# Kernel tuning notes

Hardware: AMD Instinct MI355X
Metric: run time of the kernel (lower is better)

## Reference

```python
import jax, jax.numpy as jnp
import numpy as np

# SLAYER neuron / simulation hyperparameters (from network.yaml)
THETA = 10.0      # spike threshold
TAU_SR = 10.0     # SRM (PSP) kernel time constant [ms]
TAU_REF = 1.0     # refractory kernel time constant [ms]
SCALE_REF = 2.0   # refractory kernel scale
TS = 1.0          # simulation step [ms]
K_SRM = 100       # truncation length of SRM kernel (eps decays ~0 by 10*tau)
K_REF = 32        # truncation length of refractory kernel (tauRef=1 -> decays fast)


def _eps_kernel(tau, k):
    # eps(t) = (t/tau) * exp(1 - t/tau), eps(0) = 0  (SLAYER SRM alpha kernel)
    t = jnp.arange(k, dtype=jnp.float32) * TS
    return (t / tau) * jnp.exp(1.0 - t / tau)


def psp(x, kern):
    # Causal temporal filter: y[..., t] = sum_j kern[j] * x[..., t - j]
    B, N, T = x.shape
    lhs = x.reshape(B * N, 1, T)
    rhs = kern[::-1].reshape(1, 1, -1)  # lax.conv is cross-correlation -> flip
    y = jax.lax.conv_general_dilated(
        lhs, rhs, window_strides=(1,), padding=[(kern.shape[0] - 1, 0)],
        dimension_numbers=('NCH', 'OIH', 'NCH'))
    return y.reshape(B, N, T)


def spike(u, refk):
    # Sequential thresholding with refractory feedback (SLAYER spikeFunction fwd).
    # u: [B, N, T] membrane drive. State r: future refractory contributions.
    kr = refk.shape[0]
    refk_shift = jnp.concatenate([refk[1:], jnp.zeros((1,), refk.dtype)])

    def step(r, u_t):
        m = u_t + r[..., 0]                      # membrane potential at t
        s = (m >= THETA).astype(u_t.dtype)       # hard spike
        r_next = jnp.concatenate([r[..., 1:], jnp.zeros_like(r[..., :1])], -1) \
                 + s[..., None] * refk_shift     # add refractory response
        return r_next, s

    uT = jnp.moveaxis(u, -1, 0)                  # [T, B, N]
    r0 = jnp.zeros(uT.shape[1:] + (kr,), u.dtype)
    _, sT = jax.lax.scan(step, r0, uT)
    return jnp.moveaxis(sT, 0, -1) / TS          # [B, N, T]


def setup_inputs() -> dict:
    key = jax.random.key(0)
    k1, k2, k3 = jax.random.split(key, 3)
    B, NIN, NHID, NOUT, T = 32, 2048, 512, 10, 350
    spike_input = (jax.random.uniform(k1, (B, NIN, T)) < 0.05).astype(jnp.float32)
    W1 = jax.random.normal(k2, (NHID, NIN), dtype=jnp.float32) * 0.05
    W2 = jax.random.normal(k3, (NOUT, NHID), dtype=jnp.float32) * 0.05
    return {"spike_input": spike_input, "W1": W1, "W2": W2}


def reference(spike_input, W1, W2):
    srm = _eps_kernel(TAU_SR, K_SRM)
    refk = -SCALE_REF * THETA * _eps_kernel(TAU_REF, K_REF)
    # layer 1: psp -> dense -> spike
    a1 = jnp.einsum('bnt,mn->bmt', psp(spike_input, srm), W1)
    s1 = spike(a1, refk)
    # layer 2: psp -> dense -> spike
    a2 = jnp.einsum('bnt,mn->bmt', psp(s1, srm), W2)
    s2 = spike(a2, refk)
    return s2
```

## Files before the change

### kernel.cpp

```cpp
#include <hip/hip_runtime.h>
#include <stdint.h>

static constexpr int B  = 32;
static constexpr int T  = 350;
static constexpr int NIN = 2048;
static constexpr int NH  = 512;
static constexpr int NO  = 10;
static constexpr int BT  = B * T;

static constexpr float THETA = 10.0f;
static constexpr float BETA  = 0.36787944117144233f;
static constexpr float CREF  = 54.365636569180904707f;

static constexpr size_t OFF_W1T  = 0;
static constexpr size_t OFF_MASK = 4196352;
static constexpr size_t OFF_SRM  = 7063552;
static constexpr size_t OFF_Z1   = 7064576;
static constexpr size_t OFF_A1   = 30002176;
static constexpr size_t OFF_Z2   = OFF_A1;

__global__ void __launch_bounds__(256) k_prep(const float* __restrict__ x,
                                              const float* __restrict__ W1,
                                              float* __restrict__ W1T,
                                              uint64_t* __restrict__ mask,
                                              float* __restrict__ srm28) {
    int bid = blockIdx.x;
    if (bid < 1024) {
        __shared__ uint64_t tb[6][64];
        int b = bid >> 5, nblk = bid & 31;
        int wv = threadIdx.x >> 6, lane = threadIdx.x & 63;
        for (int nr = wv; nr < 64; nr += 4) {
            const float* xp = x + ((size_t)b * NIN + nblk * 64 + nr) * T;
            #pragma unroll
            for (int c = 0; c < 6; ++c) {
                int t = c * 64 + lane;
                float v = (t < T) ? xp[t] : 0.f;
                uint64_t mk = __ballot(v != 0.0f);
                if (lane == 0) tb[c][nr] = mk;
            }
        }
        __syncthreads();
        static const uint64_t AM[6] = {
            0x00000000FFFFFFFFull, 0x0000FFFF0000FFFFull, 0x00FF00FF00FF00FFull,
            0x0F0F0F0F0F0F0F0Full, 0x3333333333333333ull, 0x5555555555555555ull };
        for (int c = wv; c < 6; c += 4) {
            uint64_t w = tb[c][lane];
            #pragma unroll
            for (int i = 0; i < 6; ++i) {
                int s = 32 >> i;
                uint64_t A = AM[i];
                uint64_t y = __shfl_xor((unsigned long long)w, s);
                if ((lane & s) == 0) w = (w & A)  | ((y & A) << s);
                else                 w = (w & ~A) | ((y & ~A) >> s);
            }
            int t = c * 64 + lane;
            if (t < T) mask[((size_t)b * T + t) * 32 + nblk] = w;
        }
    } else if (bid < 2048) {
        __shared__ float tile[32][33];
        int idx = bid - 1024;
        int n0 = (idx & 63) * 32, m0 = (idx >> 6) * 32;
        int tx = threadIdx.x & 31, ty0 = threadIdx.x >> 5;
        #pragma unroll
        for (int i = 0; i < 4; ++i) {
            int ty = ty0 + 8 * i;
            tile[ty][tx] = W1[(size_t)(m0 + ty) * NIN + n0 + tx];
        }
        __syncthreads();
        #pragma unroll
        for (int i = 0; i < 4; ++i) {
            int ty = ty0 + 8 * i;
            W1T[(size_t)(n0 + ty) * NH + m0 + tx] = tile[tx][ty];
        }
    } else {
        int j = threadIdx.x;
        if (j < 192) {
            float v = 0.f;
            int i = j - 28;
            if (i >= 0 && i < 100) { float t = (float)i; v = (t * 0.1f) * expf(1.f - t * 0.1f); }
            srm28[j] = v;
        }
        for (int i = j; i < NH; i += 256) W1T[(size_t)2048 * NH + i] = 0.f;
    }
}

__global__ void __launch_bounds__(64) k_z1(const uint64_t* __restrict__ mask,
                                           const float* __restrict__ W1T,
                                           float* __restrict__ z1) {
    __shared__ alignas(8) uint16_t lst[288];
    int row = blockIdx.x, lane = threadIdx.x;
    const uint64_t* mrow = mask + (size_t)row * 32;
    uint64_t w = (lane < 32) ? mrow[lane] : 0ull;
    int cnt = __popcll(w);
    int pre = cnt;
    #pragma unroll
    for (int off = 1; off < 64; off <<= 1) {
        int v = __shfl_up(pre, off);
        if (lane >= off) pre += v;
    }
    int total = __shfl(pre, 63);
    int excl = pre - cnt;
    while (w) {
        int bit = __builtin_ctzll(w);
        w &= w - 1;
        lst[excl++] = (uint16_t)((lane << 6) + bit);
    }
    int padded = (total + 3) & ~3;
    if (lane < padded - total) lst[total + lane] = 2048;
    __syncthreads();

    const float4* W4 = (const float4*)W1T;
    float4 a0 = {0,0,0,0}, a1v = {0,0,0,0};
    int i0 = lane * 2, i1 = lane * 2 + 1;
    for (int k = 0; k < padded; k += 4) {
        ushort4 q = *(const ushort4*)(lst + k);
        const float4* p0 = W4 + (size_t)q.x * 128;
        const float4* p1 = W4 + (size_t)q.y * 128;
        const float4* p2 = W4 + (size_t)q.z * 128;
        const float4* p3 = W4 + (size_t)q.w * 128;
        float4 x0 = p0[i0], y0 = p0[i1];
        float4 x1 = p1[i0], y1 = p1[i1];
        float4 x2 = p2[i0], y2 = p2[i1];
        float4 x3 = p3[i0], y3 = p3[i1];
        a0.x += x0.x; a0.y += x0.y; a0.z += x0.z; a0.w += x0.w;
        a1v.x += y0.x; a1v.y += y0.y; a1v.z += y0.z; a1v.w += y0.w;
        a0.x += x1.x; a0.y += x1.y; a0.z += x1.z; a0.w += x1.w;
        a1v.x += y1.x; a1v.y += y1.y; a1v.z += y1.z; a1v.w += y1.w;
        a0.x += x2.x; a0.y += x2.y; a0.z += x2.z; a0.w += x2.w;
        a1v.x += y2.x; a1v.y += y2.y; a1v.z += y2.z; a1v.w += y2.w;
        a0.x += x3.x; a0.y += x3.y; a0.z += x3.z; a0.w += x3.w;
        a1v.x += y3.x; a1v.y += y3.y; a1v.z += y3.z; a1v.w += y3.w;
    }
    float4* zp = (float4*)(z1 + (size_t)row * NH);
    zp[i0] = a0; zp[i1] = a1v;
}

__global__ void __launch_bounds__(64) k_fir1(const float* __restrict__ src,
                                             float* __restrict__ dst,
                                             const float* __restrict__ srm28) {
    __shared__ float tb[192];
    int b = blockIdx.x, half = blockIdx.y, tg = blockIdx.z;
    int lane = threadIdx.x;
    for (int i = lane; i < 192; i += 64) tb[i] = srm28[i];
    __syncthreads();
    int t0 = tg * 16;
    int m = half * 256 + lane * 4;
    const float* sp = src + (size_t)b * T * NH + m;

    float4 acc[16];
    #pragma unroll
    for (int r = 0; r < 16; ++r) acc[r] = make_float4(0.f, 0.f, 0.f, 0.f);
    float c[16];
    #pragma unroll
    for (int r = 0; r < 16; ++r) c[r] = tb[r + 127];

    for (int o = 0; o < 8; ++o) {
        #pragma unroll
        for (int j = 0; j < 16; ++j) {
            int dd = o * 16 + j;
            int tau = t0 - 99 + dd;
            float4 v = make_float4(0.f, 0.f, 0.f, 0.f);
            if (tau >= 0 && tau < T) v = *(const float4*)(sp + (size_t)tau * NH);
            #pragma unroll
            for (int r = 0; r < 16; ++r) {
                acc[r].x += c[r] * v.x; acc[r].y += c[r] * v.y;
                acc[r].z += c[r] * v.z; acc[r].w += c[r] * v.w;
            }
            #pragma unroll
            for (int r = 15; r > 0; --r) c[r] = c[r - 1];
            int ci = 126 - dd;
            c[0] = tb[ci < 0 ? 0 : ci];
        }
    }
    #pragma unroll
    for (int r = 0; r < 16; ++r) {
        int t = t0 + r;
        if (t < T) *(float4*)(dst + ((size_t)b * T + t) * NH + m) = acc[r];
    }
}

template<int M, int LAYOUT_TM>
__global__ void k_scan_t(const float* __restrict__ u, float* __restrict__ s) {
    constexpr int CT = 16;
    constexpr int NC = (T + CT - 1) / CT;
    int tid = blockIdx.x * blockDim.x + threadIdx.x;
    if (tid >= B * M) return;
    int b = tid / M, m = tid - b * M;
    const float* up = u + (size_t)b * T * M + m;
    float cur[CT], nxt[CT];
    float A = 0.f, Bs = 0.f;
    #pragma unroll
    for (int j = 0; j < CT; ++j) cur[j] = up[(size_t)j * M];
    for (int c = 0; c < NC; ++c) {
        int t0 = c * CT;
        int nsteps = (T - t0 < CT) ? (T - t0) : CT;
        if (c + 1 < NC) {
            int t1 = t0 + CT;
            #pragma unroll
            for (int j = 0; j < CT; ++j) {
                int t = t1 + j;
                nxt[j] = (t < T) ? up[(size_t)t * M] : 0.f;
            }
        }
        float outbuf[CT];
        #pragma unroll
        for (int j = 0; j < CT; ++j) {
            if (j < nsteps) {
                float mem = cur[j] - CREF * Bs;
                float sp = (mem >= THETA) ? 1.0f : 0.0f;
                A = sp + BETA * A;
                Bs = BETA * (Bs + A);
                if (LAYOUT_TM) s[((size_t)b * T + (t0 + j)) * M + m] = sp;
                else           outbuf[j] = sp;
            }
        }
        if (!LAYOUT_TM) {
            #pragma unroll
            for (int j = 0; j < CT; ++j)
                if (j < nsteps) s[((size_t)(b * M + m)) * T + t0 + j] = outbuf[j];
        }
        #pragma unroll
        for (int j = 0; j < CT; ++j) cur[j] = nxt[j];
    }
}

__global__ void __launch_bounds__(64) k_z2(const float* __restrict__ s1,
                                           const float* __restrict__ W2,
                                           float* __restrict__ z2) {
    int row = blockIdx.x;
    int lane = threadIdx.x;
    const float* sp = s1 + (size_t)row * NH;
    float acc[NO];
    #pragma unroll
    for (int o = 0; o < NO; ++o) acc[o] = 0.f;
    for (int j = 0; j < 8; ++j) {
        int m = lane + 64 * j;
        float sv = sp[m];
        #pragma unroll
        for (int o = 0; o < NO; ++o) acc[o] += sv * W2[(size_t)o * NH + m];
    }
    #pragma unroll
    for (int o = 0; o < NO; ++o) {
        float v = acc[o];
        for (int off = 32; off > 0; off >>= 1) v += __shfl_down(v, off);
        if (lane == 0) z2[(size_t)row * NO + o] = v;
    }
}

__global__ void __launch_bounds__(256) k_fir2scan(const float* __restrict__ z2,
                                                  const float* __restrict__ srm28,
                                                  float* __restrict__ out) {
    __shared__ float tb[192];
    __shared__ float zb[350 * 11 + 16];
    __shared__ float ab[352 * 10];
    int b = blockIdx.x, tid = threadIdx.x;
    if (tid < 192) tb[tid] = srm28[tid];
    const float* zp = z2 + (size_t)b * T * NO;
    for (int i = tid; i < T * NO; i += 256) {
        int t = i / NO, o = i - t * NO;
        zb[t * 11 + o] = zp[i];
    }
    __syncthreads();
    if (tid < 220) {
        int tt = tid / 10, o = tid - tt * 10;
        int t0 = tt * 16;
        float acc[16];
        #pragma unroll
        for (int r = 0; r < 16; ++r) acc[r] = 0.f;
        float c[16];
        #pragma unroll
        for (int r = 0; r < 16; ++r) c[r] = tb[r + 127];
        for (int oo = 0; oo < 8; ++oo) {
            #pragma unroll
            for (int j = 0; j < 16; ++j) {
                int dd = oo * 16 + j;
                int tau = t0 - 99 + dd;
                float v = (tau >= 0 && tau < T) ? zb[tau * 11 + o] : 0.f;
                #pragma unroll
                for (int r = 0; r < 16; ++r) acc[r] += c[r] * v;
                #pragma unroll
                for (int r = 15; r > 0; --r) c[r] = c[r - 1];
                int ci = 126 - dd;
                c[0] = tb[ci < 0 ? 0 : ci];
            }
        }
        #pragma unroll
        for (int r = 0; r < 16; ++r) {
            int t = t0 + r;
            if (t < T) ab[t * 10 + o] = acc[r];
        }
    }
    __syncthreads();
    if (tid < NO) {
        int o = tid;
        float A = 0.f, Bs = 0.f;
        float* op = out + ((size_t)b * NO + o) * T;
        for (int t = 0; t < T; ++t) {
            float mem = ab[t * 10 + o] - CREF * Bs;
            float sp = (mem >= THETA) ? 1.0f : 0.0f;
            A = sp + BETA * A;
            Bs = BETA * (Bs + A);
            op[t] = sp;
        }
    }
}

extern "C" void kernel_launch(void* const* d_in, const int* in_sizes, int n_in,
                              void* d_out, int out_size, void* d_ws, size_t ws_size,
                              hipStream_t stream) {
    const float* x  = (const float*)d_in[0];
    const float* W1 = (const float*)d_in[1];
    const float* W2 = (const float*)d_in[2];
    char* ws = (char*)d_ws;
    float*    W1T  = (float*)(ws + OFF_W1T);
    uint64_t* mask = (uint64_t*)(ws + OFF_MASK);
    float*    srm  = (float*)(ws + OFF_SRM);
    float*    z1   = (float*)(ws + OFF_Z1);
    float*    a1   = (float*)(ws + OFF_A1);
    float*    s1   = z1;
    float*    z2   = (float*)(ws + OFF_Z2);
    float*    out  = (float*)d_out;

    hipLaunchKernelGGL(k_prep,            dim3(2049),         dim3(256), 0, stream, x, W1, W1T, mask, srm);
    hipLaunchKernelGGL(k_z1,              dim3(BT),           dim3(64),  0, stream, mask, W1T, z1);
    hipLaunchKernelGGL(k_fir1,            dim3(B, 2, 22),     dim3(64),  0, stream, z1, a1, srm);
    hipLaunchKernelGGL((k_scan_t<NH, 1>), dim3((B*NH)/64),    dim3(64),  0, stream, a1, s1);
    hipLaunchKernelGGL(k_z2,              dim3(BT),           dim3(64),  0, stream, s1, W2, z2);
    hipLaunchKernelGGL(k_fir2scan,        dim3(B),            dim3(256), 0, stream, z2, srm, out);
}
```

Measured before the change: 342.9 us.

## Restructure sparse layer-1 matmul to reuse weight rows across 16 timesteps

The bit-transposed per-timestep mask and per-row gather-list sparse matmul are replaced. The prep kernel now stores raw 64-timestep ballot words per input neuron. The new k_z1 block walks all 2048 inputs, and each wave handles 16 timesteps with 16 float2 accumulators. A weight row is loaded once when any of the wave's 16 timesteps has a spike, then added into each active timestep's accumulator. This is meant to cut redundant W1T traffic, but it adds a serial scan over all 2048 inputs per block, divergent switch-based accumulation, and only 768 blocks of parallelism.

```diff
diff --git a/kernel.cpp b/kernel.cpp
--- a/kernel.cpp
+++ b/kernel.cpp
@@ -12,17 +12,17 @@
 static constexpr float BETA  = 0.36787944117144233f;
 static constexpr float CREF  = 54.365636569180904707f;
 
-static constexpr size_t OFF_W1T  = 0;
-static constexpr size_t OFF_MASK = 4196352;
-static constexpr size_t OFF_SRM  = 7063552;
-static constexpr size_t OFF_Z1   = 7064576;
-static constexpr size_t OFF_A1   = 30002176;
-static constexpr size_t OFF_Z2   = OFF_A1;
+static constexpr size_t OFF_W1T   = 0;
+static constexpr size_t OFF_SRM   = 4194304;
+static constexpr size_t OFF_Z1    = 4195328;
+static constexpr size_t OFF_A1    = 27132928;
+static constexpr size_t OFF_MASKT = OFF_A1;
+static constexpr size_t OFF_Z2    = OFF_A1;
 
 __global__ void __launch_bounds__(256) k_prep(const float* __restrict__ x,
                                               const float* __restrict__ W1,
                                               float* __restrict__ W1T,
-                                              uint64_t* __restrict__ mask,
+                                              uint64_t* __restrict__ maskt,
                                               float* __restrict__ srm28) {
     int bid = blockIdx.x;
     if (bid < 1024) {
@@ -40,21 +40,9 @@
             }
         }
         __syncthreads();
-        static const uint64_t AM[6] = {
-            0x00000000FFFFFFFFull, 0x0000FFFF0000FFFFull, 0x00FF00FF00FF00FFull,
-            0x0F0F0F0F0F0F0F0Full, 0x3333333333333333ull, 0x5555555555555555ull };
-        for (int c = wv; c < 6; c += 4) {
-            uint64_t w = tb[c][lane];
-            #pragma unroll
-            for (int i = 0; i < 6; ++i) {
-                int s = 32 >> i;
-                uint64_t A = AM[i];
-                uint64_t y = __shfl_xor((unsigned long long)w, s);
-                if ((lane & s) == 0) w = (w & A)  | ((y & A) << s);
-                else                 w = (w & ~A) | ((y & ~A) >> s);
-            }
-            int t = c * 64 + lane;
-            if (t < T) mask[((size_t)b * T + t) * 32 + nblk] = w;
+        for (int i = threadIdx.x; i < 6 * 64; i += 256) {
+            int c = i >> 6, nr = i & 63;
+            maskt[((size_t)b * 6 + c) * 2048 + nblk * 64 + nr] = tb[c][nr];
         }
     } else if (bid < 2048) {
         __shared__ float tile[32][33];
@@ -80,59 +68,75 @@
             if (i >= 0 && i < 100) { float t = (float)i; v = (t * 0.1f) * expf(1.f - t * 0.1f); }
             srm28[j] = v;
         }
-        for (int i = j; i < NH; i += 256) W1T[(size_t)2048 * NH + i] = 0.f;
-    }
-}
-
-__global__ void __launch_bounds__(64) k_z1(const uint64_t* __restrict__ mask,
-                                           const float* __restrict__ W1T,
-                                           float* __restrict__ z1) {
-    __shared__ alignas(8) uint16_t lst[288];
-    int row = blockIdx.x, lane = threadIdx.x;
-    const uint64_t* mrow = mask + (size_t)row * 32;
-    uint64_t w = (lane < 32) ? mrow[lane] : 0ull;
-    int cnt = __popcll(w);
-    int pre = cnt;
-    #pragma unroll
-    for (int off = 1; off < 64; off <<= 1) {
-        int v = __shfl_up(pre, off);
-        if (lane >= off) pre += v;
-    }
-    int total = __shfl(pre, 63);
-    int excl = pre - cnt;
-    while (w) {
-        int bit = __builtin_ctzll(w);
-        w &= w - 1;
-        lst[excl++] = (uint16_t)((lane << 6) + bit);
-    }
-    int padded = (total + 3) & ~3;
-    if (lane < padded - total) lst[total + lane] = 2048;
+    }
+}
+
+__global__ void __launch_bounds__(256) k_z1(const uint64_t* __restrict__ maskt,
+                                            const float* __restrict__ W1T,
+                                            float* __restrict__ z1) {
+    __shared__ uint64_t sm[2048];
+    int blk = blockIdx.x;
+    int mq = blk & 3;
+    int c  = (blk >> 2) % 6;
+    int b  = blk / 24;
+    int wv = threadIdx.x >> 6, lane = threadIdx.x & 63;
+    const uint64_t* mp = maskt + ((size_t)b * 6 + c) * 2048;
+    for (int i = threadIdx.x; i < 2048; i += 256) sm[i] = mp[i];
     __syncthreads();
 
-    const float4* W4 = (const float4*)W1T;
-    float4 a0 = {0,0,0,0}, a1v = {0,0,0,0};
-    int i0 = lane * 2, i1 = lane * 2 + 1;
-    for (int k = 0; k < padded; k += 4) {
-        ushort4 q = *(const ushort4*)(lst + k);
-        const float4* p0 = W4 + (size_t)q.x * 128;
-        const float4* p1 = W4 + (size_t)q.y * 128;
-        const float4* p2 = W4 + (size_t)q.z * 128;
-        const float4* p3 = W4 + (size_t)q.w * 128;
-        float4 x0 = p0[i0], y0 = p0[i1];
-        float4 x1 = p1[i0], y1 = p1[i1];
-        float4 x2 = p2[i0], y2 = p2[i1];
-        float4 x3 = p3[i0], y3 = p3[i1];
-        a0.x += x0.x; a0.y += x0.y; a0.z += x0.z; a0.w += x0.w;
-        a1v.x += y0.x; a1v.y += y0.y; a1v.z += y0.z; a1v.w += y0.w;
-        a0.x += x1.x; a0.y += x1.y; a0.z += x1.z; a0.w += x1.w;
-        a1v.x += y1.x; a1v.y += y1.y; a1v.z += y1.z; a1v.w += y1.w;
-        a0.x += x2.x; a0.y += x2.y; a0.z += x2.z; a0.w += x2.w;
-        a1v.x += y2.x; a1v.y += y2.y; a1v.z += y2.z; a1v.w += y2.w;
-        a0.x += x3.x; a0.y += x3.y; a0.z += x3.z; a0.w += x3.w;
-        a1v.x += y3.x; a1v.y += y3.y; a1v.z += y3.z; a1v.w += y3.w;
-    }
-    float4* zp = (float4*)(z1 + (size_t)row * NH);
-    zp[i0] = a0; zp[i1] = a1v;
+    int sh = wv * 16;
+    int t0 = c * 64 + sh;
+    if (t0 >= T) return;
+    int m0 = mq * 128 + lane * 2;
+    const float* Wp = W1T + m0;
+
+    float2 acc[16];
+    #pragma unroll
+    for (int r = 0; r < 16; ++r) acc[r] = make_float2(0.f, 0.f);
+
+    for (int n8 = 0; n8 < 2048; n8 += 8) {
+        uint32_t f[8];
+        #pragma unroll
+        for (int j = 0; j < 8; ++j)
+            f[j] = (uint32_t)((sm[n8 + j] >> sh) & 0xFFFFu);
+        float2 w[8];
+        #pragma unroll
+        for (int j = 0; j < 8; ++j)
+            if (f[j]) w[j] = *(const float2*)(Wp + (size_t)(n8 + j) * NH);
+        #pragma unroll
+        for (int j = 0; j < 8; ++j) {
+            uint32_t fj = f[j];
+            if (!fj) continue;
+            float2 wj = w[j];
+            while (fj) {
+                int r = __builtin_ctz(fj);
+                fj &= fj - 1;
+                switch (r) {
+                    case 0:  acc[0].x  += wj.x; acc[0].y  += wj.y; break;
+                    case 1:  acc[1].x  += wj.x; acc[1].y  += wj.y; break;
+                    case 2:  acc[2].x  += wj.x; acc[2].y  += wj.y; break;
+                    case 3:  acc[3].x  += wj.x; acc[3].y  += wj.y; break;
+                    case 4:  acc[4].x  += wj.x; acc[4].y  += wj.y; break;
+                    case 5:  acc[5].x  += wj.x; acc[5].y  += wj.y; break;
+                    case 6:  acc[6].x  += wj.x; acc[6].y  += wj.y; break;
+                    case 7:  acc[7].x  += wj.x; acc[7].y  += wj.y; break;
+                    case 8:  acc[8].x  += wj.x; acc[8].y  += wj.y; break;
+                    case 9:  acc[9].x  += wj.x; acc[9].y  += wj.y; break;
+                    case 10: acc[10].x += wj.x; acc[10].y += wj.y; break;
+                    case 11: acc[11].x += wj.x; acc[11].y += wj.y; break;
+                    case 12: acc[12].x += wj.x; acc[12].y += wj.y; break;
+                    case 13: acc[13].x += wj.x; acc[13].y += wj.y; break;
+                    case 14: acc[14].x += wj.x; acc[14].y += wj.y; break;
+                    default: acc[15].x += wj.x; acc[15].y += wj.y; break;
+                }
+            }
+        }
+    }
+    #pragma unroll
+    for (int r = 0; r < 16; ++r) {
+        int t = t0 + r;
+        if (t < T) *(float2*)(z1 + ((size_t)b * T + t) * NH + m0) = acc[r];
+    }
 }
 
 __global__ void __launch_bounds__(64) k_fir1(const float* __restrict__ src,
@@ -312,19 +316,19 @@
     const float* W1 = (const float*)d_in[1];
     const float* W2 = (const float*)d_in[2];
     char* ws = (char*)d_ws;
-    float*    W1T  = (float*)(ws + OFF_W1T);
-    uint64_t* mask = (uint64_t*)(ws + OFF_MASK);
-    float*    srm  = (float*)(ws + OFF_SRM);
-    float*    z1   = (float*)(ws + OFF_Z1);
-    float*    a1   = (float*)(ws + OFF_A1);
-    float*    s1   = z1;
-    float*    z2   = (float*)(ws + OFF_Z2);
-    float*    out  = (float*)d_out;
-
-    hipLaunchKernelGGL(k_prep,            dim3(2049),         dim3(256), 0, stream, x, W1, W1T, mask, srm);
-    hipLaunchKernelGGL(k_z1,              dim3(BT),           dim3(64),  0, stream, mask, W1T, z1);
-    hipLaunchKernelGGL(k_fir1,            dim3(B, 2, 22),     dim3(64),  0, stream, z1, a1, srm);
-    hipLaunchKernelGGL((k_scan_t<NH, 1>), dim3((B*NH)/64),    dim3(64),  0, stream, a1, s1);
-    hipLaunchKernelGGL(k_z2,              dim3(BT),           dim3(64),  0, stream, s1, W2, z2);
-    hipLaunchKernelGGL(k_fir2scan,        dim3(B),            dim3(256), 0, stream, z2, srm, out);
-}
+    float*    W1T   = (float*)(ws + OFF_W1T);
+    float*    srm   = (float*)(ws + OFF_SRM);
+    float*    z1    = (float*)(ws + OFF_Z1);
+    float*    a1    = (float*)(ws + OFF_A1);
+    uint64_t* maskt = (uint64_t*)(ws + OFF_MASKT);
+    float*    s1    = z1;
+    float*    z2    = (float*)(ws + OFF_Z2);
+    float*    out   = (float*)d_out;
+
+    hipLaunchKernelGGL(k_prep,            dim3(2049),       dim3(256), 0, stream, x, W1, W1T, maskt, srm);
+    hipLaunchKernelGGL(k_z1,              dim3(768),        dim3(256), 0, stream, maskt, W1T, z1);
+    hipLaunchKernelGGL(k_fir1,            dim3(B, 2, 22),   dim3(64),  0, stream, z1, a1, srm);
+    hipLaunchKernelGGL((k_scan_t<NH, 1>), dim3((B*NH)/64),  dim3(64),  0, stream, a1, s1);
+    hipLaunchKernelGGL(k_z2,              dim3(BT),         dim3(64),  0, stream, s1, W2, z2);
+    hipLaunchKernelGGL(k_fir2scan,        dim3(B),          dim3(256), 0, stream, z2, srm, out);
+}
```

New measurement: 833.7 us. 2.43x slower.

## Fuse layer-1 spike scan with sparse W2 projection and batch input loads in prep

Applied to the files above, without the earlier changes.

Merges the layer-1 threshold scan and the layer-2 dense projection into one kernel. Spikes are ballot-packed into shared-memory bitmasks per 16-step chunk, and only the weights of neurons that fired are summed. This removes the s1 round trip through global memory and one launch. The cost is a grid of only 32 blocks of 512 threads, which reduces parallelism for the serial scan, and a block-wide sync per chunk. Separately, k_prep now issues all loads for four rows before doing the ballots, to increase memory-level parallelism.

```diff
diff --git a/kernel.cpp b/kernel.cpp
--- a/kernel.cpp
+++ b/kernel.cpp
@@ -17,7 +17,7 @@
 static constexpr size_t OFF_SRM  = 7063552;
 static constexpr size_t OFF_Z1   = 7064576;
 static constexpr size_t OFF_A1   = 30002176;
-static constexpr size_t OFF_Z2   = OFF_A1;
+static constexpr size_t OFF_Z2   = OFF_Z1;
 
 __global__ void __launch_bounds__(256) k_prep(const float* __restrict__ x,
                                               const float* __restrict__ W1,
@@ -29,14 +29,26 @@
         __shared__ uint64_t tb[6][64];
         int b = bid >> 5, nblk = bid & 31;
         int wv = threadIdx.x >> 6, lane = threadIdx.x & 63;
-        for (int nr = wv; nr < 64; nr += 4) {
-            const float* xp = x + ((size_t)b * NIN + nblk * 64 + nr) * T;
-            #pragma unroll
-            for (int c = 0; c < 6; ++c) {
-                int t = c * 64 + lane;
-                float v = (t < T) ? xp[t] : 0.f;
-                uint64_t mk = __ballot(v != 0.0f);
-                if (lane == 0) tb[c][nr] = mk;
+        for (int g = 0; g < 4; ++g) {
+            float v[4][6];
+            #pragma unroll
+            for (int i = 0; i < 4; ++i) {
+                int nr = wv + 4 * (4 * g + i);
+                const float* xp = x + ((size_t)b * NIN + nblk * 64 + nr) * T;
+                #pragma unroll
+                for (int c = 0; c < 6; ++c) {
+                    int t = c * 64 + lane;
+                    v[i][c] = (t < T) ? xp[t] : 0.f;
+                }
+            }
+            #pragma unroll
+            for (int i = 0; i < 4; ++i) {
+                int nr = wv + 4 * (4 * g + i);
+                #pragma unroll
+                for (int c = 0; c < 6; ++c) {
+                    uint64_t mk = __ballot(v[i][c] != 0.0f);
+                    if (lane == 0) tb[c][nr] = mk;
+                }
             }
         }
         __syncthreads();
@@ -179,30 +191,32 @@
     }
 }
 
-template<int M, int LAYOUT_TM>
-__global__ void k_scan_t(const float* __restrict__ u, float* __restrict__ s) {
+__global__ void __launch_bounds__(512) k_scanz2(const float* __restrict__ a1,
+                                                const float* __restrict__ W2,
+                                                float* __restrict__ z2) {
+    __shared__ float w2s[NO * NH];
+    __shared__ uint64_t smask[16][8];
     constexpr int CT = 16;
     constexpr int NC = (T + CT - 1) / CT;
-    int tid = blockIdx.x * blockDim.x + threadIdx.x;
-    if (tid >= B * M) return;
-    int b = tid / M, m = tid - b * M;
-    const float* up = u + (size_t)b * T * M + m;
+    int b = blockIdx.x, tid = threadIdx.x;
+    int wv = tid >> 6;
+    for (int i = tid; i < NO * NH; i += 512) w2s[i] = W2[i];
+    const float* up = a1 + (size_t)b * T * NH + tid;
+    float A = 0.f, Bs = 0.f;
     float cur[CT], nxt[CT];
-    float A = 0.f, Bs = 0.f;
-    #pragma unroll
-    for (int j = 0; j < CT; ++j) cur[j] = up[(size_t)j * M];
+    #pragma unroll
+    for (int j = 0; j < CT; ++j) cur[j] = up[(size_t)j * NH];
+    __syncthreads();
     for (int c = 0; c < NC; ++c) {
         int t0 = c * CT;
         int nsteps = (T - t0 < CT) ? (T - t0) : CT;
         if (c + 1 < NC) {
-            int t1 = t0 + CT;
             #pragma unroll
             for (int j = 0; j < CT; ++j) {
-                int t = t1 + j;
-                nxt[j] = (t < T) ? up[(size_t)t * M] : 0.f;
-            }
-        }
-        float outbuf[CT];
+                int t = t0 + CT + j;
+                nxt[j] = (t < T) ? up[(size_t)t * NH] : 0.f;
+            }
+        }
         #pragma unroll
         for (int j = 0; j < CT; ++j) {
             if (j < nsteps) {
@@ -210,40 +224,30 @@
                 float sp = (mem >= THETA) ? 1.0f : 0.0f;
                 A = sp + BETA * A;
                 Bs = BETA * (Bs + A);
-                if (LAYOUT_TM) s[((size_t)b * T + (t0 + j)) * M + m] = sp;
-                else           outbuf[j] = sp;
-            }
-        }
-        if (!LAYOUT_TM) {
-            #pragma unroll
-            for (int j = 0; j < CT; ++j)
-                if (j < nsteps) s[((size_t)(b * M + m)) * T + t0 + j] = outbuf[j];
-        }
+                uint64_t mk = __ballot(sp != 0.0f);
+                if ((tid & 63) == 0) smask[j][wv] = mk;
+            }
+        }
+        __syncthreads();
+        if (tid < nsteps * NO) {
+            int j = tid / NO, o = tid - j * NO;
+            const float* wrow = w2s + o * NH;
+            float acc = 0.f;
+            #pragma unroll
+            for (int w8 = 0; w8 < 8; ++w8) {
+                uint64_t mk = smask[j][w8];
+                int base = w8 * 64;
+                while (mk) {
+                    int bit = __builtin_ctzll(mk);
+                    mk &= mk - 1;
+                    acc += wrow[base + bit];
+                }
+            }
+            z2[((size_t)b * T + t0 + j) * NO + o] = acc;
+        }
+        __syncthreads();
         #pragma unroll
         for (int j = 0; j < CT; ++j) cur[j] = nxt[j];
-    }
-}
-
-__global__ void __launch_bounds__(64) k_z2(const float* __restrict__ s1,
-                                           const float* __restrict__ W2,
-                                           float* __restrict__ z2) {
-    int row = blockIdx.x;
-    int lane = threadIdx.x;
-    const float* sp = s1 + (size_t)row * NH;
-    float acc[NO];
-    #pragma unroll
-    for (int o = 0; o < NO; ++o) acc[o] = 0.f;
-    for (int j = 0; j < 8; ++j) {
-        int m = lane + 64 * j;
-        float sv = sp[m];
-        #pragma unroll
-        for (int o = 0; o < NO; ++o) acc[o] += sv * W2[(size_t)o * NH + m];
-    }
-    #pragma unroll
-    for (int o = 0; o < NO; ++o) {
-        float v = acc[o];
-        for (int off = 32; off > 0; off >>= 1) v += __shfl_down(v, off);
-        if (lane == 0) z2[(size_t)row * NO + o] = v;
     }
 }
 
@@ -317,14 +321,12 @@
     float*    srm  = (float*)(ws + OFF_SRM);
     float*    z1   = (float*)(ws + OFF_Z1);
     float*    a1   = (float*)(ws + OFF_A1);
-    float*    s1   = z1;
     float*    z2   = (float*)(ws + OFF_Z2);
     float*    out  = (float*)d_out;
 
-    hipLaunchKernelGGL(k_prep,            dim3(2049),         dim3(256), 0, stream, x, W1, W1T, mask, srm);
-    hipLaunchKernelGGL(k_z1,              dim3(BT),           dim3(64),  0, stream, mask, W1T, z1);
-    hipLaunchKernelGGL(k_fir1,            dim3(B, 2, 22),     dim3(64),  0, stream, z1, a1, srm);
-    hipLaunchKernelGGL((k_scan_t<NH, 1>), dim3((B*NH)/64),    dim3(64),  0, stream, a1, s1);
-    hipLaunchKernelGGL(k_z2,              dim3(BT),           dim3(64),  0, stream, s1, W2, z2);
-    hipLaunchKernelGGL(k_fir2scan,        dim3(B),            dim3(256), 0, stream, z2, srm, out);
-}
+    hipLaunchKernelGGL(k_prep,     dim3(2049),     dim3(256), 0, stream, x, W1, W1T, mask, srm);
+    hipLaunchKernelGGL(k_z1,       dim3(BT),       dim3(64),  0, stream, mask, W1T, z1);
+    hipLaunchKernelGGL(k_fir1,     dim3(B, 2, 22), dim3(64),  0, stream, z1, a1, srm);
+    hipLaunchKernelGGL(k_scanz2,   dim3(B),        dim3(512), 0, stream, a1, W2, z2);
+    hipLaunchKernelGGL(k_fir2scan, dim3(B),        dim3(256), 0, stream, z2, srm, out);
+}
```

Measured after the change: 323.2 us. 5.7% less time.
